# Performance work log

Hardware: AMD Instinct MI355X
Metric: run time of the kernel (lower is better)

## Reference

```python
import jax, jax.numpy as jnp
import numpy as np

DEPTH = 4  # 2**DEPTH - 1 = 15 decision nodes, 2**DEPTH = 16 leaves


def setup_inputs() -> dict:
    key = jax.random.key(0)
    k1, k2, k3, k4, k5 = jax.random.split(key, 5)
    B, S, H = 2, 2048, 1024
    n_dec, n_leaf = 2 ** DEPTH - 1, 2 ** DEPTH
    s = 1.0 / np.sqrt(H)
    return {
        "x": jax.random.normal(k1, (B, S, H), dtype=jnp.float32),
        "Wd": jax.random.normal(k2, (n_dec, H, 2), dtype=jnp.float32) * s,
        "bd": jax.random.normal(k3, (n_dec, 2), dtype=jnp.float32) * s,
        "Wl": jax.random.normal(k4, (n_leaf, H, H), dtype=jnp.float32) * s,
        "bl": jax.random.normal(k5, (n_leaf, H), dtype=jnp.float32) * s,
    }


def reference(x, Wd, bd, Wl, bl):
    B, S, H = x.shape
    # All decision nodes in one grouped GEMM: [B,S,n_dec,2], independent sigmoids
    decisions = jax.nn.sigmoid(jnp.einsum('bsh,nhk->bsnk', x, Wd) + bd)
    # Cumulative path probabilities with torch-faithful cat([p*left, p*right]) ordering
    path = jnp.ones((B, S, 1), dtype=x.dtype)
    for level in range(DEPTH):
        start = 2 ** level - 1
        lv = decisions[:, :, start:start + 2 ** level, :]  # [B,S,2^level,2]
        path = jnp.concatenate([path * lv[..., 0], path * lv[..., 1]], axis=-1)
    # Weighted leaf-output sum without materializing [B,S,n_leaf,H]
    out = jnp.einsum('bsh,lhd,bsl->bsd', x, Wl, path, optimize=True)
    out = out + jnp.einsum('bsl,ld->bsd', path, bl)
    return out
```

## Files before the change

kernel.cpp:

```cpp
#include <hip/hip_runtime.h>
#include <hip/hip_bf16.h>

typedef unsigned short u16;
typedef unsigned int u32;
typedef short bf16x8 __attribute__((ext_vector_type(8)));
typedef _Float16 f16x8 __attribute__((ext_vector_type(8)));
typedef float f32x4 __attribute__((ext_vector_type(4)));

__device__ __forceinline__ u16 f2bf(float f) {
    u32 u = __builtin_bit_cast(u32, f);
    u32 r = (u + 0x7FFFu + ((u >> 16) & 1u)) >> 16;
    return (u16)r;
}
__device__ __forceinline__ u16 f2h(float f) {
    _Float16 h = (_Float16)f;
    return __builtin_bit_cast(u16, h);
}
__device__ __forceinline__ float h2f(u16 u) {
    return (float)__builtin_bit_cast(_Float16, u);
}

__device__ __forceinline__ void lds16(const void* g, void* s) {
    __builtin_amdgcn_global_load_lds(
        (const __attribute__((address_space(1))) u32*)g,
        (__attribute__((address_space(3))) u32*)s, 16, 0, 0);
}

__global__ __launch_bounds__(256) void pre_kernel(
    const float* __restrict__ x, const float* __restrict__ Wd,
    const float* __restrict__ bd, const float* __restrict__ Wl,
    float* __restrict__ path, u16* __restrict__ xb, u16* __restrict__ wlt,
    int as_f16, int M) {
    __shared__ float tile[64][65];
    const int bid = blockIdx.x;

    if (bid < 4096) {
        int nb = bid & 15, hb = (bid >> 4) & 15, l = bid >> 8;
        int t = threadIdx.x;
        int r = t >> 2, cq = (t & 3) << 4;

        const float* src = Wl + ((size_t)(l * 1024 + hb * 64 + r)) * 1024 + nb * 64 + cq;
#pragma unroll
        for (int j = 0; j < 4; ++j) {
            float4 w = ((const float4*)src)[j];
            tile[r][cq + 4 * j + 0] = w.x;
            tile[r][cq + 4 * j + 1] = w.y;
            tile[r][cq + 4 * j + 2] = w.z;
            tile[r][cq + 4 * j + 3] = w.w;
        }
        __syncthreads();
        union { u16 u[16]; uint4 q[2]; } pk;
#pragma unroll
        for (int j = 0; j < 16; ++j)
            pk.u[j] = as_f16 ? f2h(tile[cq + j][r]) : f2bf(tile[cq + j][r]);
        u16* dst = wlt + ((size_t)(l * 1024 + nb * 64 + r)) * 1024 + hb * 64 + cq;
        ((uint4*)dst)[0] = pk.q[0];
        ((uint4*)dst)[1] = pk.q[1];
        return;
    }

    int lane = threadIdx.x & 63;
    int wid = threadIdx.x >> 6;
    int m = (bid - 4096) * 4 + wid;
    if (m >= M) return;

    const float* xr = x + (size_t)m * 1024;
    float v[16];
#pragma unroll
    for (int i = 0; i < 16; ++i) v[i] = xr[lane + 64 * i];
#pragma unroll
    for (int i = 0; i < 16; ++i)
        xb[(size_t)m * 1024 + lane + 64 * i] = as_f16 ? f2h(v[i]) : f2bf(v[i]);

    int leaf = lane & 15;
    int nd[4], bit[4];
#pragma unroll
    for (int k = 0; k < 4; ++k) {
        nd[k] = (1 << k) - 1 + (leaf & ((1 << k) - 1));
        bit[k] = (leaf >> k) & 1;
    }
    float z[4] = {0.f, 0.f, 0.f, 0.f};

    const float2* Wd2 = (const float2*)Wd;
    for (int n = 0; n < 15; ++n) {
        float s0 = 0.f, s1 = 0.f;
#pragma unroll
        for (int i = 0; i < 16; ++i) {
            float2 w = Wd2[n * 1024 + lane + 64 * i];
            s0 += v[i] * w.x;
            s1 += v[i] * w.y;
        }
#pragma unroll
        for (int off = 32; off; off >>= 1) {
            s0 += __shfl_xor(s0, off, 64);
            s1 += __shfl_xor(s1, off, 64);
        }
#pragma unroll
        for (int k = 0; k < 4; ++k)
            if (nd[k] == n) z[k] = bit[k] ? s1 : s0;
    }
    float p = 1.f;
#pragma unroll
    for (int k = 0; k < 4; ++k) {
        float zz = z[k] + bd[nd[k] * 2 + bit[k]];
        p *= 1.f / (1.f + expf(-zz));
    }
    if (lane < 16) path[(size_t)m * 16 + leaf] = p;
}

__global__ __launch_bounds__(512, 2) void tree_gemm8(
    const u16* __restrict__ xh, const u16* __restrict__ wlt,
    const float* __restrict__ path, float* __restrict__ out,
    u16* __restrict__ part16, int M) {
    __shared__ __align__(16) u16 Asm[2][2][128 * 64];
    __shared__ __align__(16) u16 Bsm[2][2][128 * 64];
    __shared__ u16 psm_h[4][256];

    const int tid = threadIdx.x, lane = tid & 63, w = tid >> 6;
    const int wm = w >> 2, wn = w & 3;
    const int nbm = M >> 8;
    int xb_, yb_, zb_;
    {
        int bid = blockIdx.x;
        if ((nbm << 4) == 256) {
            int k = bid & 7, s = bid >> 3;
            zb_ = k >> 1; yb_ = (k & 1) * 8 + (s >> 2); xb_ = s & 3;
        } else {
            xb_ = bid & 3; int t2 = bid >> 2; yb_ = t2 % nbm; zb_ = t2 / nbm;
        }
    }
    const int n0 = xb_ * 256, m0 = yb_ * 256, z = zb_;
    const int z4 = z * 4;
    const int rl = lane >> 3;
    const int srcswz = ((lane & 7) ^ rl) << 4;
    const int arow = (lane & 15) * 128;
    const int coff0 = ((lane >> 4) << 4) ^ ((lane & 7) << 4);

    for (int i = tid; i < 1024; i += 512) {
        int r = i >> 2, lz = i & 3;
        psm_h[lz][r] = f2h(path[(size_t)(m0 + r) * 16 + z4 + lz]);
    }

#define ISSUE_A(dst_, ks_)                                                          \
    {                                                                               \
        _Pragma("unroll") for (int h_ = 0; h_ < 2; ++h_)                            \
        _Pragma("unroll") for (int j_ = 0; j_ < 2; ++j_)                            \
            lds16((const char*)xh +                                                 \
                      (size_t)(m0 + h_ * 128 + w * 16 + j_ * 8 + rl) * 2048 +       \
                      ((ks_) << 7) + srcswz,                                        \
                  (dst_) + h_ * 16384 + w * 2048 + j_ * 1024);                      \
    }
#define ISSUE_B(dst_, t_)                                                           \
    if ((t_) < 64) {                                                                \
        size_t lb_ = (size_t)(z4 + ((t_) & 3)) * 2097152 +                          \
                     ((size_t)((t_) >> 2) << 7);                                    \
        _Pragma("unroll") for (int h_ = 0; h_ < 2; ++h_)                            \
        _Pragma("unroll") for (int j_ = 0; j_ < 2; ++j_)                            \
            lds16((const char*)wlt + lb_ +                                          \
                      (size_t)(n0 + h_ * 128 + w * 16 + j_ * 8 + rl) * 2048 +       \
                      srcswz,                                                       \
                  (dst_) + h_ * 16384 + w * 2048 + j_ * 1024);                      \
    }
#define LDA4(aB_, mfb)                                                              \
    _Pragma("unroll") for (int q_ = 0; q_ < 4; ++q_) {                              \
        aR[q_][0] = *(const f16x8*)((aB_) + ((mfb) + q_) * 2048 + coff0);           \
        aR[q_][1] = *(const f16x8*)((aB_) + ((mfb) + q_) * 2048 + (coff0 ^ 64));    \
    }
#define LDB2(bB_, nfb, d0)                                                          \
    _Pragma("unroll") for (int q_ = 0; q_ < 2; ++q_) {                              \
        bR[(d0) + q_][0] = *(const f16x8*)((bB_) + ((nfb) + q_) * 2048 + coff0);    \
        bR[(d0) + q_][1] =                                                          \
            *(const f16x8*)((bB_) + ((nfb) + q_) * 2048 + (coff0 ^ 64));            \
    }
#define LDP(ll, mfb)                                                                \
    _Pragma("unroll") for (int q_ = 0; q_ < 4; ++q_)                                \
        p2[q_] = __builtin_bit_cast(                                                \
            _Float16, psm_h[ll][wm * 128 + ((mfb) + q_) * 16 + (lane & 15)]);
#define SCALE                                                                       \
    _Pragma("unroll") for (int q_ = 0; q_ < 4; ++q_) {                              \
        aR[q_][0] *= p2[q_];                                                        \
        aR[q_][1] *= p2[q_];                                                        \
    }
#define MM(a0, b0)                                                                  \
    _Pragma("unroll") for (int mq_ = 0; mq_ < 4; ++mq_)                             \
    _Pragma("unroll") for (int nq_ = 0; nq_ < 2; ++nq_) {                           \
        acc[(a0) + mq_][(b0) + nq_] = __builtin_amdgcn_mfma_f32_16x16x32_f16(       \
            aR[mq_][0], bR[(b0) + nq_][0], acc[(a0) + mq_][(b0) + nq_], 0, 0, 0);   \
        acc[(a0) + mq_][(b0) + nq_] = __builtin_amdgcn_mfma_f32_16x16x32_f16(       \
            aR[mq_][1], bR[(b0) + nq_][1], acc[(a0) + mq_][(b0) + nq_], 0, 0, 0);   \
    }
#define BAR __builtin_amdgcn_s_barrier()
#define SCHED0 __builtin_amdgcn_sched_barrier(0)
#define PRIO1 __builtin_amdgcn_s_setprio(1)
#define PRIO0 __builtin_amdgcn_s_setprio(0)
#define VM0 asm volatile("s_waitcnt vmcnt(0)" ::: "memory")
#define VM4 asm volatile("s_waitcnt vmcnt(4)" ::: "memory")
#define NOPX ((void)0)

#define TILE(aB_, bB_, ll, EB, EA, WT)                                              \
    {                                                                               \
        f16x8 aR[4][2], bR[4][2];                                                   \
        _Float16 p2[4];                                                             \
        LDA4(aB_, 0); LDB2(bB_, 0, 0); LDB2(bB_, 2, 2); LDP(ll, 0);                 \
        EB; EA;                                                                     \
        SCALE;                                                                      \
        PRIO1; MM(0, 0); MM(0, 2); PRIO0;                                           \
        LDA4(aB_, 4); LDP(ll, 4);                                                   \
        SCALE;                                                                      \
        PRIO1; MM(4, 0); MM(4, 2); PRIO0;                                           \
        WT; BAR;                                                                    \
    }

    f32x4 acc[8][4];
#pragma unroll
    for (int a = 0; a < 8; ++a)
#pragma unroll
        for (int b = 0; b < 4; ++b) acc[a][b] = (f32x4){0.f, 0.f, 0.f, 0.f};

    const char* aBase0 = (const char*)Asm[0][wm] + arow;
    const char* aBase1 = (const char*)Asm[1][wm] + arow;
    const char* bBase0 = (const char*)Bsm[0][wn >> 1] + (wn & 1) * 8192 + arow;
    const char* bBase1 = (const char*)Bsm[1][wn >> 1] + (wn & 1) * 8192 + arow;
    char* aSlot0 = (char*)Asm[0][0];
    char* aSlot1 = (char*)Asm[1][0];
    char* bSlot0 = (char*)Bsm[0][0];
    char* bSlot1 = (char*)Bsm[1][0];

    ISSUE_A(aSlot0, 0);
    ISSUE_B(bSlot0, 0);
    asm volatile("s_waitcnt vmcnt(0) lgkmcnt(0)" ::: "memory");
    BAR;
    SCHED0;

#pragma unroll 1
    for (int ks = 0; ks < 15; ++ks) {
        const int t4 = ks << 2;
        const char* aB = (ks & 1) ? aBase1 : aBase0;
        char* aD = (ks & 1) ? aSlot0 : aSlot1;
        TILE(aB, bBase0, 0, ISSUE_B(bSlot1, t4 + 1), NOPX, VM0);
        TILE(aB, bBase1, 1, ISSUE_B(bSlot0, t4 + 2), ISSUE_A(aD, ks + 1), VM4);
        TILE(aB, bBase0, 2, ISSUE_B(bSlot1, t4 + 3), NOPX, VM0);
        TILE(aB, bBase1, 3, ISSUE_B(bSlot0, t4 + 4), NOPX, VM0);
    }
    {
        const char* aB = aBase1;
        TILE(aB, bBase0, 0, ISSUE_B(bSlot1, 61), NOPX, VM0);
        TILE(aB, bBase1, 1, ISSUE_B(bSlot0, 62), NOPX, VM0);
        TILE(aB, bBase0, 2, ISSUE_B(bSlot1, 63), NOPX, VM0);
        TILE(aB, bBase1, 3, NOPX, NOPX, NOPX);
    }

    const int r0 = m0 + wm * 128 + ((lane >> 4) << 2);
    const int c0 = n0 + wn * 64 + (lane & 15);
    if (z == 0) {
#pragma unroll
        for (int mf = 0; mf < 8; ++mf)
#pragma unroll
            for (int jj = 0; jj < 4; ++jj)
#pragma unroll
                for (int nf = 0; nf < 4; ++nf)
                    out[(size_t)(r0 + mf * 16 + jj) * 1024 + c0 + nf * 16] =
                        acc[mf][nf][jj];
    } else {
        u16* po = part16 + (size_t)(z - 1) * M * 1024;
#pragma unroll
        for (int mf = 0; mf < 8; ++mf)
#pragma unroll
            for (int jj = 0; jj < 4; ++jj)
#pragma unroll
                for (int nf = 0; nf < 4; ++nf)
                    po[(size_t)(r0 + mf * 16 + jj) * 1024 + c0 + nf * 16] =
                        f2h(acc[mf][nf][jj]);
    }
#undef ISSUE_A
#undef ISSUE_B
#undef LDA4
#undef LDB2
#undef LDP
#undef SCALE
#undef MM
#undef BAR
#undef SCHED0
#undef PRIO1
#undef PRIO0
#undef VM0
#undef VM4
#undef NOPX
#undef TILE
}

__global__ __launch_bounds__(256) void tree_gemm_fb(
    const u16* __restrict__ xb, const u16* __restrict__ wlt,
    const float* __restrict__ path, float* __restrict__ pout,
    int M, int LPB, int lgLPB) {
    __shared__ __align__(16) u16 Asm[128 * 64];
    __shared__ __align__(16) u16 Bsm[128 * 64];
    __shared__ float psm[128][16];

    const int tid = threadIdx.x, lane = tid & 63, wid = tid >> 6;
    const int wm = wid >> 1, wn = wid & 1;
    const int m0 = blockIdx.y * 128, n0 = blockIdx.x * 128;
    const int lbase = blockIdx.z * LPB;

    for (int i = tid; i < (128 << lgLPB); i += 256) {
        int r = i >> lgLPB, c = i & (LPB - 1);
        psm[r][c] = path[(size_t)(m0 + r) * 16 + lbase + c];
    }

    const int colb = (((lane & 7) ^ (lane >> 3)) << 4);
    const int rl = lane >> 3;

    f32x4 accF[4][4], accL[4][4];
#pragma unroll
    for (int a = 0; a < 4; ++a)
#pragma unroll
        for (int b = 0; b < 4; ++b) {
            accF[a][b] = (f32x4){0.f, 0.f, 0.f, 0.f};
            accL[a][b] = (f32x4){0.f, 0.f, 0.f, 0.f};
        }

    const int nsteps = LPB << 4;
    for (int sl = 0; sl < nsteps; ++sl) {
        const int l_ = lbase + (sl >> 4);
        const int h2_ = (sl & 15) << 7;
#pragma unroll
        for (int i_ = 0; i_ < 4; ++i_) {
            int seg_ = wid * 4 + i_;
            int r_ = seg_ * 8 + rl;
            lds16((const char*)xb + (size_t)(m0 + r_) * 2048 + h2_ + colb,
                  (char*)Asm + seg_ * 1024);
            lds16((const char*)wlt + (size_t)(l_ * 1024 + n0 + r_) * 2048 + h2_ + colb,
                  (char*)Bsm + seg_ * 1024);
        }
        __syncthreads();

#pragma unroll
        for (int kf = 0; kf < 2; ++kf) {
            int c2 = kf * 64 + ((lane >> 4) << 4);
            bf16x8 af[4], bfr[4];
#pragma unroll
            for (int mf = 0; mf < 4; ++mf) {
                int rr = wm * 64 + mf * 16 + (lane & 15);
                af[mf] = *(const bf16x8*)((const char*)Asm + rr * 128 + (c2 ^ ((lane & 7) << 4)));
            }
#pragma unroll
            for (int nf = 0; nf < 4; ++nf) {
                int rr = wn * 64 + nf * 16 + (lane & 15);
                bfr[nf] = *(const bf16x8*)((const char*)Bsm + rr * 128 + (c2 ^ ((lane & 7) << 4)));
            }
#pragma unroll
            for (int mf = 0; mf < 4; ++mf)
#pragma unroll
                for (int nf = 0; nf < 4; ++nf)
                    accL[mf][nf] = __builtin_amdgcn_mfma_f32_16x16x32_bf16(
                        af[mf], bfr[nf], accL[mf][nf], 0, 0, 0);
        }
        __syncthreads();

        if ((sl & 15) == 15) {
            int ll = sl >> 4;
#pragma unroll
            for (int mf = 0; mf < 4; ++mf)
#pragma unroll
                for (int jj = 0; jj < 4; ++jj) {
                    float p = psm[wm * 64 + mf * 16 + ((lane >> 4) << 2) + jj][ll];
#pragma unroll
                    for (int nf = 0; nf < 4; ++nf) {
                        accF[mf][nf][jj] += p * accL[mf][nf][jj];
                        accL[mf][nf][jj] = 0.f;
                    }
                }
        }
    }

    float* po = pout + (size_t)blockIdx.z * M * 1024;
#pragma unroll
    for (int mf = 0; mf < 4; ++mf)
#pragma unroll
        for (int jj = 0; jj < 4; ++jj) {
            int rowl = wm * 64 + mf * 16 + ((lane >> 4) << 2) + jj;
#pragma unroll
            for (int nf = 0; nf < 4; ++nf) {
                int col = n0 + wn * 64 + nf * 16 + (lane & 15);
                po[(size_t)(m0 + rowl) * 1024 + col] = accF[mf][nf][jj];
            }
        }
}

__global__ __launch_bounds__(256) void reduce_kernel(
    const void* __restrict__ extra, const float* __restrict__ path,
    const float* __restrict__ bl, float* __restrict__ out, int M,
    int nExtra, int readOut, int ext16) {
    int m = blockIdx.x, t = threadIdx.x;
    size_t i4 = (size_t)m * 256 + t;
    f32x4 acc = {0.f, 0.f, 0.f, 0.f};
    if (readOut) acc = ((const f32x4*)out)[i4];
    if (ext16) {
        const ushort4* e = (const ushort4*)extra;
        for (int g = 0; g < nExtra; ++g) {
            ushort4 v = e[(size_t)g * M * 256 + i4];
            acc[0] += h2f(v.x);
            acc[1] += h2f(v.y);
            acc[2] += h2f(v.z);
            acc[3] += h2f(v.w);
        }
    } else {
        const f32x4* e = (const f32x4*)extra;
        for (int g = 0; g < nExtra; ++g) acc += e[(size_t)g * M * 256 + i4];
    }
#pragma unroll
    for (int l = 0; l < 16; ++l) {
        float p = path[(size_t)m * 16 + l];
        f32x4 b = ((const f32x4*)bl)[l * 256 + t];
        acc += p * b;
    }
    ((f32x4*)out)[i4] = acc;
}

extern "C" void kernel_launch(void* const* d_in, const int* in_sizes, int n_in,
                              void* d_out, int out_size, void* d_ws, size_t ws_size,
                              hipStream_t stream) {
    const float* x  = (const float*)d_in[0];
    const float* Wd = (const float*)d_in[1];
    const float* bd = (const float*)d_in[2];
    const float* Wl = (const float*)d_in[3];
    const float* bl = (const float*)d_in[4];
    float* out = (float*)d_out;

    const int H = 1024;
    const int M = in_sizes[0] / H;
    char* ws = (char*)d_ws;

    size_t n_off_xh   = (size_t)M * 16 * 4;
    size_t n_off_wlt  = n_off_xh + (size_t)M * 1024 * 2;
    size_t n_off_part = n_off_wlt + (size_t)16 * 1024 * 1024 * 2;
    size_t n_need     = n_off_part + 3 * (size_t)M * 1024 * 2;

    if (ws_size >= n_need && (M % 256) == 0) {
        float* path = (float*)ws;
        u16* xh  = (u16*)(ws + n_off_xh);
        u16* wlt = (u16*)(ws + n_off_wlt);
        u16* part16 = (u16*)(ws + n_off_part);

        pre_kernel<<<4096 + M / 4, 256, 0, stream>>>(x, Wd, bd, Wl, path, xh, wlt, 1, M);
        tree_gemm8<<<4 * (M / 256) * 4, 512, 0, stream>>>(xh, wlt, path, out, part16, M);
        reduce_kernel<<<M, 256, 0, stream>>>(part16, path, bl, out, M, 3, 1, 1);
        return;
    }

    size_t off_xb   = (size_t)M * 16 * 4;
    size_t off_wlt  = off_xb + (size_t)M * 1024 * 2;
    size_t off_part = off_wlt + (size_t)16 * 1024 * 1024 * 2;
    size_t per_part = (size_t)M * 1024 * 4;

    int G = 1;
    if (ws_size >= off_part + 4 * per_part) G = 4;
    else if (ws_size >= off_part + 2 * per_part) G = 2;
    const int LPB = 16 / G;
    const int lgLPB = (G == 1) ? 4 : (G == 2) ? 3 : 2;

    float* path = (float*)ws;
    u16* xb  = (u16*)(ws + off_xb);
    u16* wlt = (u16*)(ws + off_wlt);
    float* pout = (G == 1) ? out : (float*)(ws + off_part);

    pre_kernel<<<4096 + (M + 3) / 4, 256, 0, stream>>>(x, Wd, bd, Wl, path, xb, wlt, 0, M);
    tree_gemm_fb<<<dim3(8, M / 128, G), 256, 0, stream>>>(xb, wlt, path, pout, M, LPB, lgLPB);
    reduce_kernel<<<M, 256, 0, stream>>>(pout, path, bl, out, M,
                                         (G == 1) ? 0 : G, (G == 1) ? 1 : 0, 0);
}
```

Before: 199.3 us.

## Double waves per block in tree GEMM, shrinking per-wave tile to 64x64

Grows the tree_gemm8 block from 8 to 16 waves on the same 256x256 output tile, so each wave computes a 64x64 sub-tile instead of 128x64. Each wave now issues half as many global-to-LDS copies per stage, adjusts the vmcnt wait and fragment addressing, and holds half as many accumulators. The aim is more waves per CU to hide LDS and global latency, since the 128 KB shared footprint likely allows only one block per CU. The trade-off is lower register reuse: each wave reads more fragment bytes from LDS per MFMA. The tighter launch-bounds hint also caps registers per thread.

```diff
diff --git a/kernel.cpp b/kernel.cpp
--- a/kernel.cpp
+++ b/kernel.cpp
@@ -108,7 +108,7 @@
     if (lane < 16) path[(size_t)m * 16 + leaf] = p;
 }
 
-__global__ __launch_bounds__(512, 2) void tree_gemm8(
+__global__ __launch_bounds__(1024, 4) void tree_gemm8(
     const u16* __restrict__ xh, const u16* __restrict__ wlt,
     const float* __restrict__ path, float* __restrict__ out,
     u16* __restrict__ part16, int M) {
@@ -133,94 +133,86 @@
     const int z4 = z * 4;
     const int rl = lane >> 3;
     const int srcswz = ((lane & 7) ^ rl) << 4;
-    const int arow = (lane & 15) * 128;
+    const int frow = lane & 15;
     const int coff0 = ((lane >> 4) << 4) ^ ((lane & 7) << 4);
 
-    for (int i = tid; i < 1024; i += 512) {
-        int r = i >> 2, lz = i & 3;
+    {
+        int r = tid >> 2, lz = tid & 3;
         psm_h[lz][r] = f2h(path[(size_t)(m0 + r) * 16 + z4 + lz]);
     }
 
 #define ISSUE_A(dst_, ks_)                                                          \
     {                                                                               \
         _Pragma("unroll") for (int h_ = 0; h_ < 2; ++h_)                            \
-        _Pragma("unroll") for (int j_ = 0; j_ < 2; ++j_)                            \
             lds16((const char*)xh +                                                 \
-                      (size_t)(m0 + h_ * 128 + w * 16 + j_ * 8 + rl) * 2048 +       \
+                      (size_t)(m0 + h_ * 128 + w * 8 + rl) * 2048 +                 \
                       ((ks_) << 7) + srcswz,                                        \
-                  (dst_) + h_ * 16384 + w * 2048 + j_ * 1024);                      \
+                  (dst_) + h_ * 16384 + w * 1024);                                  \
     }
 #define ISSUE_B(dst_, t_)                                                           \
     if ((t_) < 64) {                                                                \
         size_t lb_ = (size_t)(z4 + ((t_) & 3)) * 2097152 +                          \
                      ((size_t)((t_) >> 2) << 7);                                    \
         _Pragma("unroll") for (int h_ = 0; h_ < 2; ++h_)                            \
-        _Pragma("unroll") for (int j_ = 0; j_ < 2; ++j_)                            \
             lds16((const char*)wlt + lb_ +                                          \
-                      (size_t)(n0 + h_ * 128 + w * 16 + j_ * 8 + rl) * 2048 +       \
-                      srcswz,                                                       \
-                  (dst_) + h_ * 16384 + w * 2048 + j_ * 1024);                      \
-    }
-#define LDA4(aB_, mfb)                                                              \
-    _Pragma("unroll") for (int q_ = 0; q_ < 4; ++q_) {                              \
-        aR[q_][0] = *(const f16x8*)((aB_) + ((mfb) + q_) * 2048 + coff0);           \
-        aR[q_][1] = *(const f16x8*)((aB_) + ((mfb) + q_) * 2048 + (coff0 ^ 64));    \
-    }
-#define LDB2(bB_, nfb, d0)                                                          \
-    _Pragma("unroll") for (int q_ = 0; q_ < 2; ++q_) {                              \
-        bR[(d0) + q_][0] = *(const f16x8*)((bB_) + ((nfb) + q_) * 2048 + coff0);    \
-        bR[(d0) + q_][1] =                                                          \
-            *(const f16x8*)((bB_) + ((nfb) + q_) * 2048 + (coff0 ^ 64));            \
-    }
-#define LDP(ll, mfb)                                                                \
+                      (size_t)(n0 + h_ * 128 + w * 8 + rl) * 2048 + srcswz,         \
+                  (dst_) + h_ * 16384 + w * 1024);                                  \
+    }
+#define LDA4(aB_, co_)                                                              \
+    _Pragma("unroll") for (int q_ = 0; q_ < 4; ++q_)                                \
+        aR[q_] = *(const f16x8*)((aB_) + q_ * 2048 + (co_));
+#define LDB4(bB_, co_)                                                              \
+    _Pragma("unroll") for (int q_ = 0; q_ < 4; ++q_)                                \
+        bR[q_] = *(const f16x8*)((bB_) + q_ * 2048 + (co_));
+#define LDP(ll)                                                                     \
     _Pragma("unroll") for (int q_ = 0; q_ < 4; ++q_)                                \
         p2[q_] = __builtin_bit_cast(                                                \
-            _Float16, psm_h[ll][wm * 128 + ((mfb) + q_) * 16 + (lane & 15)]);
+            _Float16, psm_h[ll][wm * 64 + q_ * 16 + frow]);
 #define SCALE                                                                       \
-    _Pragma("unroll") for (int q_ = 0; q_ < 4; ++q_) {                              \
-        aR[q_][0] *= p2[q_];                                                        \
-        aR[q_][1] *= p2[q_];                                                        \
-    }
-#define MM(a0, b0)                                                                  \
+    _Pragma("unroll") for (int q_ = 0; q_ < 4; ++q_) aR[q_] *= p2[q_];
+#define MM16                                                                        \
     _Pragma("unroll") for (int mq_ = 0; mq_ < 4; ++mq_)                             \
-    _Pragma("unroll") for (int nq_ = 0; nq_ < 2; ++nq_) {                           \
-        acc[(a0) + mq_][(b0) + nq_] = __builtin_amdgcn_mfma_f32_16x16x32_f16(       \
-            aR[mq_][0], bR[(b0) + nq_][0], acc[(a0) + mq_][(b0) + nq_], 0, 0, 0);   \
-        acc[(a0) + mq_][(b0) + nq_] = __builtin_amdgcn_mfma_f32_16x16x32_f16(       \
-            aR[mq_][1], bR[(b0) + nq_][1], acc[(a0) + mq_][(b0) + nq_], 0, 0, 0);   \
-    }
+    _Pragma("unroll") for (int nq_ = 0; nq_ < 4; ++nq_)                             \
+        acc[mq_][nq_] = __builtin_amdgcn_mfma_f32_16x16x32_f16(                     \
+            aR[mq_], bR[nq_], acc[mq_][nq_], 0, 0, 0);
 #define BAR __builtin_amdgcn_s_barrier()
 #define SCHED0 __builtin_amdgcn_sched_barrier(0)
 #define PRIO1 __builtin_amdgcn_s_setprio(1)
 #define PRIO0 __builtin_amdgcn_s_setprio(0)
 #define VM0 asm volatile("s_waitcnt vmcnt(0)" ::: "memory")
-#define VM4 asm volatile("s_waitcnt vmcnt(4)" ::: "memory")
+#define VM2 asm volatile("s_waitcnt vmcnt(2)" ::: "memory")
 #define NOPX ((void)0)
 
 #define TILE(aB_, bB_, ll, EB, EA, WT)                                              \
     {                                                                               \
-        f16x8 aR[4][2], bR[4][2];                                                   \
         _Float16 p2[4];                                                             \
-        LDA4(aB_, 0); LDB2(bB_, 0, 0); LDB2(bB_, 2, 2); LDP(ll, 0);                 \
-        EB; EA;                                                                     \
-        SCALE;                                                                      \
-        PRIO1; MM(0, 0); MM(0, 2); PRIO0;                                           \
-        LDA4(aB_, 4); LDP(ll, 4);                                                   \
-        SCALE;                                                                      \
-        PRIO1; MM(4, 0); MM(4, 2); PRIO0;                                           \
+        LDP(ll);                                                                    \
+        {                                                                           \
+            f16x8 aR[4], bR[4];                                                     \
+            LDA4(aB_, coff0); LDB4(bB_, coff0);                                     \
+            EB; EA;                                                                 \
+            SCALE;                                                                  \
+            PRIO1; MM16; PRIO0;                                                     \
+        }                                                                           \
+        {                                                                           \
+            f16x8 aR[4], bR[4];                                                     \
+            LDA4(aB_, coff0 ^ 64); LDB4(bB_, coff0 ^ 64);                           \
+            SCALE;                                                                  \
+            PRIO1; MM16; PRIO0;                                                     \
+        }                                                                           \
         WT; BAR;                                                                    \
     }
 
-    f32x4 acc[8][4];
-#pragma unroll
-    for (int a = 0; a < 8; ++a)
+    f32x4 acc[4][4];
+#pragma unroll
+    for (int a = 0; a < 4; ++a)
 #pragma unroll
         for (int b = 0; b < 4; ++b) acc[a][b] = (f32x4){0.f, 0.f, 0.f, 0.f};
 
-    const char* aBase0 = (const char*)Asm[0][wm] + arow;
-    const char* aBase1 = (const char*)Asm[1][wm] + arow;
-    const char* bBase0 = (const char*)Bsm[0][wn >> 1] + (wn & 1) * 8192 + arow;
-    const char* bBase1 = (const char*)Bsm[1][wn >> 1] + (wn & 1) * 8192 + arow;
+    const char* aBase0 = (const char*)Asm[0][wm >> 1] + ((wm & 1) * 64 + frow) * 128;
+    const char* aBase1 = (const char*)Asm[1][wm >> 1] + ((wm & 1) * 64 + frow) * 128;
+    const char* bBase0 = (const char*)Bsm[0][wn >> 1] + ((wn & 1) * 64 + frow) * 128;
+    const char* bBase1 = (const char*)Bsm[1][wn >> 1] + ((wn & 1) * 64 + frow) * 128;
     char* aSlot0 = (char*)Asm[0][0];
     char* aSlot1 = (char*)Asm[1][0];
     char* bSlot0 = (char*)Bsm[0][0];
@@ -238,7 +230,7 @@
         const char* aB = (ks & 1) ? aBase1 : aBase0;
         char* aD = (ks & 1) ? aSlot0 : aSlot1;
         TILE(aB, bBase0, 0, ISSUE_B(bSlot1, t4 + 1), NOPX, VM0);
-        TILE(aB, bBase1, 1, ISSUE_B(bSlot0, t4 + 2), ISSUE_A(aD, ks + 1), VM4);
+        TILE(aB, bBase1, 1, ISSUE_B(bSlot0, t4 + 2), ISSUE_A(aD, ks + 1), VM2);
         TILE(aB, bBase0, 2, ISSUE_B(bSlot1, t4 + 3), NOPX, VM0);
         TILE(aB, bBase1, 3, ISSUE_B(bSlot0, t4 + 4), NOPX, VM0);
     }
@@ -250,11 +242,11 @@
         TILE(aB, bBase1, 3, NOPX, NOPX, NOPX);
     }
 
-    const int r0 = m0 + wm * 128 + ((lane >> 4) << 2);
-    const int c0 = n0 + wn * 64 + (lane & 15);
+    const int r0 = m0 + wm * 64 + ((lane >> 4) << 2);
+    const int c0 = n0 + wn * 64 + frow;
     if (z == 0) {
 #pragma unroll
-        for (int mf = 0; mf < 8; ++mf)
+        for (int mf = 0; mf < 4; ++mf)
 #pragma unroll
             for (int jj = 0; jj < 4; ++jj)
 #pragma unroll
@@ -264,7 +256,7 @@
     } else {
         u16* po = part16 + (size_t)(z - 1) * M * 1024;
 #pragma unroll
-        for (int mf = 0; mf < 8; ++mf)
+        for (int mf = 0; mf < 4; ++mf)
 #pragma unroll
             for (int jj = 0; jj < 4; ++jj)
 #pragma unroll
@@ -275,16 +267,16 @@
 #undef ISSUE_A
 #undef ISSUE_B
 #undef LDA4
-#undef LDB2
+#undef LDB4
 #undef LDP
 #undef SCALE
-#undef MM
+#undef MM16
 #undef BAR
 #undef SCHED0
 #undef PRIO1
 #undef PRIO0
 #undef VM0
-#undef VM4
+#undef VM2
 #undef NOPX
 #undef TILE
 }
@@ -443,7 +435,7 @@
         u16* part16 = (u16*)(ws + n_off_part);
 
         pre_kernel<<<4096 + M / 4, 256, 0, stream>>>(x, Wd, bd, Wl, path, xh, wlt, 1, M);
-        tree_gemm8<<<4 * (M / 256) * 4, 512, 0, stream>>>(xh, wlt, path, out, part16, M);
+        tree_gemm8<<<4 * (M / 256) * 4, 1024, 0, stream>>>(xh, wlt, path, out, part16, M);
         reduce_kernel<<<M, 256, 0, stream>>>(part16, path, bl, out, M, 3, 1, 1);
         return;
     }
```

New measurement: 215.1 us. 1.08x slower.
